# Kernel optimization log

Hardware: AMD Instinct MI355X
Metric: run time of the kernel (lower is better)

## Reference

```python
import jax, jax.numpy as jnp
import numpy as np

NUM_CLASSES = 21
THRESH = 0.5
NEGPOS = 3
VAR0, VAR1 = 0.1, 0.2
FEAT = 19
N_ANCH = 9
B = 256
NUM_OBJS = 12
P = FEAT * FEAT * N_ANCH  # 3249


def make_priors():
    # 19x19 grid, 3 scales x 3 aspect ratios (1, 2, 1/2) -> 9 anchors/cell, center form
    cxy = (np.arange(FEAT, dtype=np.float32) + 0.5) / FEAT
    cx, cy = np.meshgrid(cxy, cxy, indexing='ij')  # [19,19]
    scales = np.array([0.1, 0.2, 0.35], dtype=np.float32)
    ratios = np.array([1.0, 2.0, 0.5], dtype=np.float32)
    w = (scales[:, None] * np.sqrt(ratios)[None, :]).reshape(-1)  # [9]
    h = (scales[:, None] / np.sqrt(ratios)[None, :]).reshape(-1)
    cx = np.broadcast_to(cx[:, :, None], (FEAT, FEAT, N_ANCH))
    cy = np.broadcast_to(cy[:, :, None], (FEAT, FEAT, N_ANCH))
    w = np.broadcast_to(w[None, None, :], (FEAT, FEAT, N_ANCH))
    h = np.broadcast_to(h[None, None, :], (FEAT, FEAT, N_ANCH))
    pri = np.stack([cx, cy, w, h], axis=-1).reshape(-1, 4)
    return jnp.asarray(np.clip(pri, 1e-3, 1.0))


def setup_inputs() -> dict:
    key = jax.random.key(0)
    k1, k2, k3, k4, k5 = jax.random.split(key, 5)
    loc_data = jax.random.normal(k1, (B, P, 4), dtype=jnp.float32)
    conf_data = jax.random.normal(k2, (B, P, NUM_CLASSES), dtype=jnp.float32)
    priors = make_priors()
    xy = jax.random.uniform(k3, (B, NUM_OBJS, 2), minval=0.05, maxval=0.65)
    wh = jax.random.uniform(k4, (B, NUM_OBJS, 2), minval=0.05, maxval=0.30)
    labels = jax.random.randint(k5, (B, NUM_OBJS), 0, NUM_CLASSES - 1).astype(jnp.float32)
    targets = jnp.concatenate([xy, xy + wh, labels[..., None]], axis=-1)  # [B,O,5]
    return {"loc_data": loc_data, "conf_data": conf_data, "priors": priors, "targets": targets}


def point_form(boxes):  # (cx,cy,w,h) -> (x1,y1,x2,y2)
    return jnp.concatenate([boxes[:, :2] - boxes[:, 2:] / 2,
                            boxes[:, :2] + boxes[:, 2:] / 2], axis=1)


def jaccard(a, b):  # a: [n,4], b: [m,4] point form -> [n,m]
    lt = jnp.maximum(a[:, None, :2], b[None, :, :2])
    rb = jnp.minimum(a[:, None, 2:], b[None, :, 2:])
    inter = jnp.prod(jnp.clip(rb - lt, 0.0, None), axis=-1)
    area_a = jnp.prod(a[:, 2:] - a[:, :2], axis=-1)
    area_b = jnp.prod(b[:, 2:] - b[:, :2], axis=-1)
    return inter / (area_a[:, None] + area_b[None, :] - inter)


def encode(matched, priors):  # matched point-form [P,4], priors center-form [P,4]
    g_cxcy = ((matched[:, :2] + matched[:, 2:]) / 2 - priors[:, :2]) / (VAR0 * priors[:, 2:])
    g_wh = jnp.log((matched[:, 2:] - matched[:, :2]) / priors[:, 2:]) / VAR1
    return jnp.concatenate([g_cxcy, g_wh], axis=1)


def match_one(truths, labels, priors, priors_pt):
    overlaps = jaccard(truths, priors_pt)          # [O,P]
    best_prior_idx = jnp.argmax(overlaps, axis=1)  # [O]
    best_truth_ov = jnp.max(overlaps, axis=0)      # [P]
    best_truth_idx = jnp.argmax(overlaps, axis=0)  # [P]
    best_truth_ov = best_truth_ov.at[best_prior_idx].set(2.0)
    best_truth_idx = best_truth_idx.at[best_prior_idx].set(jnp.arange(truths.shape[0]))
    matches = truths[best_truth_idx]               # [P,4]
    conf = labels[best_truth_idx] + 1
    conf = jnp.where(best_truth_ov < THRESH, 0, conf)
    return encode(matches, priors), conf


def reference(loc_data, conf_data, priors, targets):
    truths = targets[:, :, :4]
    labels = targets[:, :, 4].astype(jnp.int32)
    priors_pt = point_form(priors)
    loc_t, conf_t = jax.vmap(lambda t, l: match_one(t, l, priors, priors_pt))(truths, labels)
    loc_t = jax.lax.stop_gradient(loc_t)
    conf_t = jax.lax.stop_gradient(conf_t)

    pos = conf_t > 0                                               # [B,P]
    # smooth L1 (sum) over matched priors
    d = loc_data - loc_t
    ad = jnp.abs(d)
    sl1 = jnp.where(ad < 1.0, 0.5 * d * d, ad - 0.5)
    loss_l = jnp.sum(sl1 * pos[..., None].astype(sl1.dtype))

    # per-prior CE = logsumexp - logit[target]
    lse = jax.nn.logsumexp(conf_data, axis=-1)                     # [B,P]
    gathered = jnp.take_along_axis(conf_data, conf_t[..., None], axis=2)[..., 0]
    ce = lse - gathered                                            # [B,P]

    # hard negative mining: double argsort rank of neg losses
    loss_c_mine = jnp.where(pos, 0.0, ce)
    loss_idx = jnp.argsort(-loss_c_mine, axis=1)
    idx_rank = jnp.argsort(loss_idx, axis=1)
    num_pos = jnp.sum(pos, axis=1, keepdims=True)                  # [B,1]
    num_neg = jnp.minimum(NEGPOS * num_pos, P - 1)
    neg = idx_rank < num_neg

    sel = pos | neg
    loss_c = jnp.sum(jnp.where(sel, ce, 0.0))

    have_centerloss = jnp.max(sel.reshape(B, FEAT, FEAT, N_ANCH), axis=3).reshape(-1)
    conf_t_featuremap = jnp.max(conf_t.reshape(B, FEAT, FEAT, N_ANCH), axis=3).reshape(-1)

    N = jnp.sum(num_pos).astype(loc_data.dtype)
    return loss_l / N, loss_c / N, conf_t_featuremap, have_centerloss
```

## Files before the change

kernel.cpp:

```cpp
#include <hip/hip_runtime.h>
#include <math.h>

#pragma clang fp contract(off)

#define BB      256
#define PP      3249
#define NCLS    21
#define NOBJ    12
#define CELLS   361
#define THRESH_ 0.5f

typedef float vf4 __attribute__((ext_vector_type(4), aligned(4)));


__global__ __launch_bounds__(1024) void fused_kernel(
    const float* __restrict__ loc, const float* __restrict__ conf,
    const float* __restrict__ priors, const float* __restrict__ targets,
    int* __restrict__ numpos, double* __restrict__ lossl,
    double* __restrict__ lossc, float* __restrict__ out)
{
    const int b = blockIdx.x, tid = threadIdx.x;
    const int lane = tid & 63, wid = tid >> 6;

    __shared__ float s_tx1[NOBJ], s_ty1[NOBJ], s_tx2[NOBJ], s_ty2[NOBJ];
    __shared__ float s_area_t[NOBJ];
    __shared__ int   s_label[NOBJ];
    __shared__ float s_bov[PP];
    __shared__ short s_bidx[PP];
    __shared__ int   s_bpi[NOBJ];
    __shared__ float s_wov[NOBJ][16];
    __shared__ int   s_widx[NOBJ][16];
    __shared__ unsigned long long s_key[PP];
    __shared__ unsigned char s_ct[PP];
    __shared__ unsigned char s_sel[PP];
    __shared__ int s_hist[256];
    __shared__ int s_chosen, s_knext, s_nneg;
    __shared__ double s_pl[16];
    __shared__ int    s_pn[16];
    __shared__ double s_pc[16];

    if (tid < NOBJ) {
        const float* t = targets + ((size_t)b * NOBJ + tid) * 5;
        float x1 = t[0], y1 = t[1], x2 = t[2], y2 = t[3];
        s_tx1[tid] = x1; s_ty1[tid] = y1; s_tx2[tid] = x2; s_ty2[tid] = y2;
        s_label[tid] = (int)t[4];
        s_area_t[tid] = (x2 - x1) * (y2 - y1);
    }
    __syncthreads();

    float l_bov[NOBJ];
    int   l_bidx[NOBJ];
#pragma unroll
    for (int j = 0; j < NOBJ; ++j) { l_bov[j] = -1.0f; l_bidx[j] = 0x7FFFFFFF; }

    for (int p = tid; p < PP; p += 1024) {
        float cx = priors[4*p+0], cy = priors[4*p+1], w = priors[4*p+2], h = priors[4*p+3];
        float px1 = cx - w / 2.0f, py1 = cy - h / 2.0f;
        float px2 = cx + w / 2.0f, py2 = cy + h / 2.0f;
        float area_p = (px2 - px1) * (py2 - py1);
        float bov = -1.0f; int bidx = 0;
#pragma unroll
        for (int j = 0; j < NOBJ; ++j) {
            float ltx = fmaxf(s_tx1[j], px1);
            float lty = fmaxf(s_ty1[j], py1);
            float rbx = fminf(s_tx2[j], px2);
            float rby = fminf(s_ty2[j], py2);
            float iw = fmaxf(rbx - ltx, 0.0f);
            float ih = fmaxf(rby - lty, 0.0f);
            float inter = iw * ih;
            float iou = inter / ((s_area_t[j] + area_p) - inter);
            if (iou > bov) { bov = iou; bidx = j; }
            if (iou > l_bov[j]) { l_bov[j] = iou; l_bidx[j] = p; }
        }
        s_bov[p] = bov;
        s_bidx[p] = (short)bidx;
    }

#pragma unroll
    for (int j = 0; j < NOBJ; ++j) {
        float ov = l_bov[j]; int ix = l_bidx[j];
#pragma unroll
        for (int off = 32; off > 0; off >>= 1) {
            float ov2 = __shfl_xor(ov, off);
            int   ix2 = __shfl_xor(ix, off);
            if (ov2 > ov || (ov2 == ov && ix2 < ix)) { ov = ov2; ix = ix2; }
        }
        if (lane == 0) { s_wov[j][wid] = ov; s_widx[j][wid] = ix; }
    }
    __syncthreads();
    if (tid < NOBJ) {
        float ov = s_wov[tid][0]; int ix = s_widx[tid][0];
#pragma unroll
        for (int w2 = 1; w2 < 16; ++w2) {
            float ov2 = s_wov[tid][w2]; int ix2 = s_widx[tid][w2];
            if (ov2 > ov || (ov2 == ov && ix2 < ix)) { ov = ov2; ix = ix2; }
        }
        s_bpi[tid] = ix;
    }
    __syncthreads();

    int my_pos = 0;
    double my_lossl = 0.0;
    const float* confb = conf + (size_t)b * PP * NCLS;
    for (int p = tid; p < PP; p += 1024) {
        int jov = -1;
#pragma unroll
        for (int j = 0; j < NOBJ; ++j) if (s_bpi[j] == p) jov = j;
        int idx; float ov;
        if (jov >= 0) { idx = jov; ov = 2.0f; }
        else          { idx = (int)s_bidx[p]; ov = s_bov[p]; }
        int c = (ov < THRESH_) ? 0 : (s_label[idx] + 1);
        s_ct[p] = (unsigned char)c;

        const float* cd = confb + (size_t)p * NCLS;
        const vf4* cd4 = (const vf4*)cd;
        float rw[NCLS];
#pragma unroll
        for (int v = 0; v < 5; ++v) {
            vf4 q = cd4[v];
            rw[4*v+0] = q[0]; rw[4*v+1] = q[1]; rw[4*v+2] = q[2]; rw[4*v+3] = q[3];
        }
        rw[20] = cd[20];

        float m = rw[0];
#pragma unroll
        for (int k = 1; k < NCLS; ++k) m = fmaxf(m, rw[k]);
        float s = 0.0f;
#pragma unroll
        for (int k = 0; k < NCLS; ++k) s += expf(rw[k] - m);
        float cdc = rw[0];
#pragma unroll
        for (int k = 1; k < NCLS; ++k) if (c == k) cdc = rw[k];
        float ce = (logf(s) + m) - cdc;

        float v = (c > 0) ? 0.0f : ce;
        s_key[p] = ((unsigned long long)__float_as_uint(v) << 32)
                 | (unsigned int)(0xFFFFFFFFu - (unsigned int)p);
        s_bov[p] = ce;

        if (c > 0) {
            ++my_pos;
            float cx = priors[4*p+0], cy = priors[4*p+1], w = priors[4*p+2], h = priors[4*p+3];
            float m0 = s_tx1[idx], m1 = s_ty1[idx], m2 = s_tx2[idx], m3 = s_ty2[idx];
            float g0 = ((m0 + m2) / 2.0f - cx) / (0.1f * w);
            float g1 = ((m1 + m3) / 2.0f - cy) / (0.1f * h);
            float g2 = logf((m2 - m0) / w) / 0.2f;
            float g3 = logf((m3 - m1) / h) / 0.2f;
            const float* ld = loc + ((size_t)b * PP + p) * 4;
            float d0 = ld[0] - g0, d1 = ld[1] - g1, d2 = ld[2] - g2, d3 = ld[3] - g3;
            float a0 = fabsf(d0), a1 = fabsf(d1), a2 = fabsf(d2), a3 = fabsf(d3);
            my_lossl += (double)((a0 < 1.0f) ? 0.5f * d0 * d0 : a0 - 0.5f);
            my_lossl += (double)((a1 < 1.0f) ? 0.5f * d1 * d1 : a1 - 0.5f);
            my_lossl += (double)((a2 < 1.0f) ? 0.5f * d2 * d2 : a2 - 0.5f);
            my_lossl += (double)((a3 < 1.0f) ? 0.5f * d3 * d3 : a3 - 0.5f);
        }
    }
#pragma unroll
    for (int off = 32; off > 0; off >>= 1) {
        my_lossl += __shfl_down(my_lossl, off);
        my_pos   += __shfl_down(my_pos, off);
    }
    if (lane == 0) { s_pl[wid] = my_lossl; s_pn[wid] = my_pos; }
    __syncthreads();
    if (tid == 0) {
        double L = 0.0; int n = 0;
#pragma unroll
        for (int w2 = 0; w2 < 16; ++w2) { L += s_pl[w2]; n += s_pn[w2]; }
        lossl[b] = L; numpos[b] = n;
        s_nneg = min(3 * n, PP - 1);
    }
    __syncthreads();

    const int ds[6] = {56, 48, 40, 32, 8, 0};
    unsigned long long prefix = 0ull, pmask = 0ull;
    int kk = s_nneg;
#pragma unroll
    for (int ri = 0; ri < 6; ++ri) {
        const int d = ds[ri];
        if (tid < 256) s_hist[tid] = 0;
        __syncthreads();
        for (int i = tid; i < PP; i += 1024) {
            unsigned long long key = s_key[i];
            if ((key & pmask) == prefix)
                atomicAdd(&s_hist[(int)((key >> d) & 0xFF)], 1);
        }
        __syncthreads();
        if (tid < 64) {
            int h0 = s_hist[4*lane+0], h1 = s_hist[4*lane+1];
            int h2 = s_hist[4*lane+2], h3 = s_hist[4*lane+3];
            int ls = h0 + h1 + h2 + h3;
            int x = ls;
#pragma unroll
            for (int off = 1; off < 64; off <<= 1) {
                int y = __shfl_down(x, off);
                if (lane + off < 64) x += y;
            }
            int excl = x - ls;
            int cb3 = excl;
            int cb2 = cb3 + h3;
            int cb1 = cb2 + h2;
            int cb0 = cb1 + h1;
            if (cb3 < kk && kk <= cb3 + h3) { s_chosen = 4*lane+3; s_knext = kk - cb3; }
            if (cb2 < kk && kk <= cb2 + h2) { s_chosen = 4*lane+2; s_knext = kk - cb2; }
            if (cb1 < kk && kk <= cb1 + h1) { s_chosen = 4*lane+1; s_knext = kk - cb1; }
            if (cb0 < kk && kk <= cb0 + h0) { s_chosen = 4*lane+0; s_knext = kk - cb0; }
        }
        __syncthreads();
        prefix |= ((unsigned long long)(unsigned int)s_chosen) << d;
        pmask  |= 0xFFull << d;
        kk = s_knext;
        if (d == 32) { prefix |= 0xFFFF0000ull; pmask |= 0xFFFF0000ull; }
        __syncthreads();
    }
    const unsigned long long kth = prefix;

    double my_c = 0.0;
    for (int p = tid; p < PP; p += 1024) {
        int c = s_ct[p];
        bool sel = (c > 0) || (s_key[p] >= kth);
        s_sel[p] = sel ? 1 : 0;
        if (sel) my_c += (double)s_bov[p];
    }
    __syncthreads();

    for (int cI = tid; cI < CELLS; cI += 1024) {
        int mc = 0, hv = 0;
#pragma unroll
        for (int a = 0; a < 9; ++a) {
            int p = cI * 9 + a;
            int cv = s_ct[p];
            mc = (cv > mc) ? cv : mc;
            hv |= s_sel[p];
        }
        out[2 + (size_t)b * CELLS + cI] = (float)mc;
        out[2 + (size_t)BB * CELLS + (size_t)b * CELLS + cI] = (float)hv;
    }

#pragma unroll
    for (int off = 32; off > 0; off >>= 1) my_c += __shfl_down(my_c, off);
    if (lane == 0) s_pc[wid] = my_c;
    __syncthreads();
    if (tid == 0) {
        double L = 0.0;
#pragma unroll
        for (int w2 = 0; w2 < 16; ++w2) L += s_pc[w2];
        lossc[b] = L;
    }
}

__global__ __launch_bounds__(256) void finalize_kernel(
    const int* __restrict__ numpos, const double* __restrict__ lossl,
    const double* __restrict__ lossc, float* __restrict__ out)
{
    __shared__ double s_l[256], s_c[256];
    __shared__ int s_n[256];
    int tid = threadIdx.x;
    s_n[tid] = numpos[tid];
    s_l[tid] = lossl[tid];
    s_c[tid] = lossc[tid];
    __syncthreads();
    for (int s = 128; s > 0; s >>= 1) {
        if (tid < s) { s_n[tid] += s_n[tid + s]; s_l[tid] += s_l[tid + s]; s_c[tid] += s_c[tid + s]; }
        __syncthreads();
    }
    if (tid == 0) {
        double N = (double)s_n[0];
        out[0] = (float)(s_l[0] / N);
        out[1] = (float)(s_c[0] / N);
    }
}

extern "C" void kernel_launch(void* const* d_in, const int* in_sizes, int n_in,
                              void* d_out, int out_size, void* d_ws, size_t ws_size,
                              hipStream_t stream) {
    const float* loc     = (const float*)d_in[0];
    const float* conf    = (const float*)d_in[1];
    const float* priors  = (const float*)d_in[2];
    const float* targets = (const float*)d_in[3];
    float* out = (float*)d_out;

    double* ws_lossl  = (double*)d_ws;
    double* ws_lossc  = ws_lossl + BB;
    int*    ws_numpos = (int*)(ws_lossc + BB);

    hipLaunchKernelGGL(fused_kernel, dim3(BB), dim3(1024), 0, stream,
                       loc, conf, priors, targets, ws_numpos, ws_lossl, ws_lossc, out);
    hipLaunchKernelGGL(finalize_kernel, dim3(1), dim3(256), 0, stream,
                       ws_numpos, ws_lossl, ws_lossc, out);
}
```

Baseline: 138.5 us.

## Split log-sum-exp into a grid-wide kernel and warp-aggregate histogram atomics

Moves the per-prior log-sum-exp over the 21 class logits out of the 256-block fused kernel into a separate kernel with one thread per prior, spread across thousands of blocks. The fused kernel then only gathers the target logit and reads the precomputed LSE. The goal is to stream the large conf tensor with much more parallelism than one block per image allows. The radix-select histogram now combines same-bin increments within a wavefront using ballots before the shared atomic, and double-buffers the histogram to drop one barrier per round. Object indices are also cached in registers. The cost is an extra launch, a workspace round trip for the LSE values, and a scattered re-read of one logit per prior.

After: 150.6 us. 1.09x slower.

```diff
diff --git a/kernel.cpp b/kernel.cpp
--- a/kernel.cpp
+++ b/kernel.cpp
@@ -13,9 +13,34 @@
 typedef float vf4 __attribute__((ext_vector_type(4), aligned(4)));
 
 
+__global__ __launch_bounds__(256) void lse_kernel(
+    const float* __restrict__ conf, float* __restrict__ lse_out)
+{
+    int idx = blockIdx.x * 256 + threadIdx.x;
+    if (idx >= BB * PP) return;
+    const float* cd = conf + (size_t)idx * NCLS;
+    const vf4* cd4 = (const vf4*)cd;
+    float rw[NCLS];
+#pragma unroll
+    for (int v = 0; v < 5; ++v) {
+        vf4 q = cd4[v];
+        rw[4*v+0] = q[0]; rw[4*v+1] = q[1]; rw[4*v+2] = q[2]; rw[4*v+3] = q[3];
+    }
+    rw[20] = cd[20];
+
+    float m = rw[0];
+#pragma unroll
+    for (int k = 1; k < NCLS; ++k) m = fmaxf(m, rw[k]);
+    float s = 0.0f;
+#pragma unroll
+    for (int k = 0; k < NCLS; ++k) s += expf(rw[k] - m);
+    lse_out[idx] = logf(s) + m;
+}
+
 __global__ __launch_bounds__(1024) void fused_kernel(
     const float* __restrict__ loc, const float* __restrict__ conf,
     const float* __restrict__ priors, const float* __restrict__ targets,
+    const float* __restrict__ lse_in,
     int* __restrict__ numpos, double* __restrict__ lossl,
     double* __restrict__ lossc, float* __restrict__ out)
 {
@@ -33,7 +58,7 @@
     __shared__ unsigned long long s_key[PP];
     __shared__ unsigned char s_ct[PP];
     __shared__ unsigned char s_sel[PP];
-    __shared__ int s_hist[256];
+    __shared__ int s_hist[2][256];
     __shared__ int s_chosen, s_knext, s_nneg;
     __shared__ double s_pl[16];
     __shared__ int    s_pn[16];
@@ -99,39 +124,27 @@
     }
     __syncthreads();
 
+    int bpi[NOBJ];
+#pragma unroll
+    for (int j = 0; j < NOBJ; ++j) bpi[j] = s_bpi[j];
+
     int my_pos = 0;
     double my_lossl = 0.0;
     const float* confb = conf + (size_t)b * PP * NCLS;
+    const float* lseb  = lse_in + (size_t)b * PP;
     for (int p = tid; p < PP; p += 1024) {
         int jov = -1;
 #pragma unroll
-        for (int j = 0; j < NOBJ; ++j) if (s_bpi[j] == p) jov = j;
+        for (int j = 0; j < NOBJ; ++j) if (bpi[j] == p) jov = j;
         int idx; float ov;
         if (jov >= 0) { idx = jov; ov = 2.0f; }
         else          { idx = (int)s_bidx[p]; ov = s_bov[p]; }
         int c = (ov < THRESH_) ? 0 : (s_label[idx] + 1);
         s_ct[p] = (unsigned char)c;
 
-        const float* cd = confb + (size_t)p * NCLS;
-        const vf4* cd4 = (const vf4*)cd;
-        float rw[NCLS];
-#pragma unroll
-        for (int v = 0; v < 5; ++v) {
-            vf4 q = cd4[v];
-            rw[4*v+0] = q[0]; rw[4*v+1] = q[1]; rw[4*v+2] = q[2]; rw[4*v+3] = q[3];
-        }
-        rw[20] = cd[20];
-
-        float m = rw[0];
-#pragma unroll
-        for (int k = 1; k < NCLS; ++k) m = fmaxf(m, rw[k]);
-        float s = 0.0f;
-#pragma unroll
-        for (int k = 0; k < NCLS; ++k) s += expf(rw[k] - m);
-        float cdc = rw[0];
-#pragma unroll
-        for (int k = 1; k < NCLS; ++k) if (c == k) cdc = rw[k];
-        float ce = (logf(s) + m) - cdc;
+        float lse = lseb[p];
+        float cdc = confb[(size_t)p * NCLS + c];
+        float ce  = lse - cdc;
 
         float v = (c > 0) ? 0.0f : ce;
         s_key[p] = ((unsigned long long)__float_as_uint(v) << 32)
@@ -161,6 +174,7 @@
         my_pos   += __shfl_down(my_pos, off);
     }
     if (lane == 0) { s_pl[wid] = my_lossl; s_pn[wid] = my_pos; }
+    if (tid < 512) ((int*)s_hist)[tid] = 0;
     __syncthreads();
     if (tid == 0) {
         double L = 0.0; int n = 0;
@@ -177,17 +191,24 @@
 #pragma unroll
     for (int ri = 0; ri < 6; ++ri) {
         const int d = ds[ri];
-        if (tid < 256) s_hist[tid] = 0;
-        __syncthreads();
+        int* hist = s_hist[ri & 1];
         for (int i = tid; i < PP; i += 1024) {
             unsigned long long key = s_key[i];
-            if ((key & pmask) == prefix)
-                atomicAdd(&s_hist[(int)((key >> d) & 0xFF)], 1);
+            bool active = ((key & pmask) == prefix);
+            unsigned bin = (unsigned)((key >> d) & 0xFF);
+            unsigned long long mm = __ballot(active);
+#pragma unroll
+            for (int bit = 0; bit < 8; ++bit) {
+                unsigned long long bb = __ballot(active && ((bin >> bit) & 1));
+                mm &= ((bin >> bit) & 1) ? bb : ~bb;
+            }
+            if (active && (__ffsll((unsigned long long)mm) - 1 == lane))
+                atomicAdd(&hist[bin], (int)__popcll(mm));
         }
         __syncthreads();
         if (tid < 64) {
-            int h0 = s_hist[4*lane+0], h1 = s_hist[4*lane+1];
-            int h2 = s_hist[4*lane+2], h3 = s_hist[4*lane+3];
+            int h0 = hist[4*lane+0], h1 = hist[4*lane+1];
+            int h2 = hist[4*lane+2], h3 = hist[4*lane+3];
             int ls = h0 + h1 + h2 + h3;
             int x = ls;
 #pragma unroll
@@ -204,13 +225,14 @@
             if (cb2 < kk && kk <= cb2 + h2) { s_chosen = 4*lane+2; s_knext = kk - cb2; }
             if (cb1 < kk && kk <= cb1 + h1) { s_chosen = 4*lane+1; s_knext = kk - cb1; }
             if (cb0 < kk && kk <= cb0 + h0) { s_chosen = 4*lane+0; s_knext = kk - cb0; }
+        } else if (tid < 64 + 256) {
+            s_hist[(ri + 1) & 1][tid - 64] = 0;
         }
         __syncthreads();
         prefix |= ((unsigned long long)(unsigned int)s_chosen) << d;
         pmask  |= 0xFFull << d;
         kk = s_knext;
         if (d == 32) { prefix |= 0xFFFF0000ull; pmask |= 0xFFFF0000ull; }
-        __syncthreads();
     }
     const unsigned long long kth = prefix;
 
@@ -282,9 +304,13 @@
     double* ws_lossl  = (double*)d_ws;
     double* ws_lossc  = ws_lossl + BB;
     int*    ws_numpos = (int*)(ws_lossc + BB);
-
+    float*  ws_lse    = (float*)(ws_numpos + BB);
+
+    hipLaunchKernelGGL(lse_kernel, dim3((BB * PP) / 256), dim3(256), 0, stream,
+                       conf, ws_lse);
     hipLaunchKernelGGL(fused_kernel, dim3(BB), dim3(1024), 0, stream,
-                       loc, conf, priors, targets, ws_numpos, ws_lossl, ws_lossc, out);
+                       loc, conf, priors, targets, ws_lse,
+                       ws_numpos, ws_lossl, ws_lossc, out);
     hipLaunchKernelGGL(finalize_kernel, dim3(1), dim3(256), 0, stream,
                        ws_numpos, ws_lossl, ws_lossc, out);
 }
```

## Overlap conf loads with IoU, shrink radix select to 32-bit keys

Applied to the files above, without the earlier changes.

Conf rows and priors are now loaded up front so their global-memory latency overlaps the IoU matching, and the per-prior logsumexp is precomputed into shared memory. The target-class logit is then gathered with a single load. The 64-bit radix select over eight 8-bit passes is replaced by a 32-bit key select using 12-bit histograms built with ballot-aggregated atomics, stopping early once the chosen bin holds a single element. Ties are resolved by a separate index pass, and selection is fused into the per-cell output loop. This adds a lot of shared memory and register pressure, which may limit occupancy.

New measurement: 141.9 us. 2.4% more time.

```diff
diff --git a/kernel.cpp b/kernel.cpp
--- a/kernel.cpp
+++ b/kernel.cpp
@@ -9,11 +9,79 @@
 #define NOBJ    12
 #define CELLS   361
 #define THRESH_ 0.5f
+#define HB      4096
 
 typedef float vf4 __attribute__((ext_vector_type(4), aligned(4)));
 
 
-__global__ __launch_bounds__(1024) void fused_kernel(
+struct Row { vf4 a, b, c, d, e; float f; };
+
+__device__ __forceinline__ Row load_row(const float* cd) {
+    const vf4* q = (const vf4*)cd;
+    Row r;
+    r.a = q[0]; r.b = q[1]; r.c = q[2]; r.d = q[3]; r.e = q[4];
+    r.f = cd[20];
+    return r;
+}
+
+__device__ __forceinline__ float lse21(const Row& r) {
+    float m = r.a[0];
+    m = fmaxf(m, r.a[1]); m = fmaxf(m, r.a[2]); m = fmaxf(m, r.a[3]);
+    m = fmaxf(m, r.b[0]); m = fmaxf(m, r.b[1]); m = fmaxf(m, r.b[2]); m = fmaxf(m, r.b[3]);
+    m = fmaxf(m, r.c[0]); m = fmaxf(m, r.c[1]); m = fmaxf(m, r.c[2]); m = fmaxf(m, r.c[3]);
+    m = fmaxf(m, r.d[0]); m = fmaxf(m, r.d[1]); m = fmaxf(m, r.d[2]); m = fmaxf(m, r.d[3]);
+    m = fmaxf(m, r.e[0]); m = fmaxf(m, r.e[1]); m = fmaxf(m, r.e[2]); m = fmaxf(m, r.e[3]);
+    m = fmaxf(m, r.f);
+    float s = 0.0f;
+    s += expf(r.a[0]-m); s += expf(r.a[1]-m); s += expf(r.a[2]-m); s += expf(r.a[3]-m);
+    s += expf(r.b[0]-m); s += expf(r.b[1]-m); s += expf(r.b[2]-m); s += expf(r.b[3]-m);
+    s += expf(r.c[0]-m); s += expf(r.c[1]-m); s += expf(r.c[2]-m); s += expf(r.c[3]-m);
+    s += expf(r.d[0]-m); s += expf(r.d[1]-m); s += expf(r.d[2]-m); s += expf(r.d[3]-m);
+    s += expf(r.e[0]-m); s += expf(r.e[1]-m); s += expf(r.e[2]-m); s += expf(r.e[3]-m);
+    s += expf(r.f-m);
+    return logf(s) + m;
+}
+
+template <int NBITS>
+__device__ __forceinline__ void scan_hist(const unsigned* key_arr, int* hist,
+                                          unsigned prefix, unsigned pmask,
+                                          int shift, int tid, int lane) {
+    for (int i = tid; i < PP; i += 1024) {
+        unsigned key = key_arr[i];
+        bool active = ((key & pmask) == prefix);
+        unsigned bin = (key >> shift) & ((1u << NBITS) - 1u);
+        unsigned long long mm = __ballot(active);
+#pragma unroll
+        for (int bit = 0; bit < NBITS; ++bit) {
+            unsigned long long bb = __ballot(active && ((bin >> bit) & 1));
+            mm &= ((bin >> bit) & 1) ? bb : ~bb;
+        }
+        if (active && (__ffsll((unsigned long long)mm) - 1 == lane))
+            atomicAdd(&hist[bin], (int)__popcll(mm));
+    }
+}
+
+__device__ __forceinline__ void pick_bin(const int* hist, int nbins, int kv, int lane,
+                                         int* s_chosen, int* s_knext, int* s_cnt) {
+    const int per = nbins >> 6;
+    const int base = lane * per;
+    int ls = 0;
+    for (int k = 0; k < per; ++k) ls += hist[base + k];
+    int x = ls;
+#pragma unroll
+    for (int off = 1; off < 64; off <<= 1) {
+        int y = __shfl_down(x, off);
+        if (lane + off < 64) x += y;
+    }
+    int cum = x - ls;
+    for (int k = per - 1; k >= 0; --k) {
+        int h = hist[base + k];
+        if (cum < kv && kv <= cum + h) { *s_chosen = base + k; *s_knext = kv - cum; *s_cnt = h; }
+        cum += h;
+    }
+}
+
+__global__ __launch_bounds__(1024, 4) void fused_kernel(
     const float* __restrict__ loc, const float* __restrict__ conf,
     const float* __restrict__ priors, const float* __restrict__ targets,
     int* __restrict__ numpos, double* __restrict__ lossl,
@@ -27,14 +95,16 @@
     __shared__ int   s_label[NOBJ];
     __shared__ float s_bov[PP];
     __shared__ short s_bidx[PP];
+    __shared__ float s_lse[PP];
+    __shared__ float s_c0[PP];
+    __shared__ unsigned s_key[PP];
+    __shared__ unsigned char s_ct[PP];
     __shared__ int   s_bpi[NOBJ];
     __shared__ float s_wov[NOBJ][16];
     __shared__ int   s_widx[NOBJ][16];
-    __shared__ unsigned long long s_key[PP];
-    __shared__ unsigned char s_ct[PP];
-    __shared__ unsigned char s_sel[PP];
-    __shared__ int s_hist[256];
-    __shared__ int s_chosen, s_knext, s_nneg;
+    __shared__ int s_hist[2][HB];
+    __shared__ int s_chosen, s_knext, s_cnt, s_nneg;
+    __shared__ unsigned s_f;
     __shared__ double s_pl[16];
     __shared__ int    s_pn[16];
     __shared__ double s_pc[16];
@@ -48,13 +118,23 @@
     }
     __syncthreads();
 
+    const float* confb = conf + (size_t)b * PP * NCLS;
+    const int p0 = tid, p1 = tid + 1024, p2 = tid + 2048, p3 = tid + 3072;
+    const bool h3 = (p3 < PP);
+
+    vf4 pr0 = *(const vf4*)(priors + 4 * p0);
+    vf4 pr1 = *(const vf4*)(priors + 4 * p1);
+    vf4 pr2 = *(const vf4*)(priors + 4 * p2);
+    vf4 pr3; if (h3) pr3 = *(const vf4*)(priors + 4 * p3);
+    Row ra = load_row(confb + (size_t)p0 * NCLS);
+
     float l_bov[NOBJ];
     int   l_bidx[NOBJ];
 #pragma unroll
     for (int j = 0; j < NOBJ; ++j) { l_bov[j] = -1.0f; l_bidx[j] = 0x7FFFFFFF; }
 
-    for (int p = tid; p < PP; p += 1024) {
-        float cx = priors[4*p+0], cy = priors[4*p+1], w = priors[4*p+2], h = priors[4*p+3];
+    auto iou_body = [&](vf4 prr, int p) {
+        float cx = prr[0], cy = prr[1], w = prr[2], h = prr[3];
         float px1 = cx - w / 2.0f, py1 = cy - h / 2.0f;
         float px2 = cx + w / 2.0f, py2 = cy + h / 2.0f;
         float area_p = (px2 - px1) * (py2 - py1);
@@ -74,7 +154,11 @@
         }
         s_bov[p] = bov;
         s_bidx[p] = (short)bidx;
-    }
+    };
+    iou_body(pr0, p0);
+    iou_body(pr1, p1);
+    iou_body(pr2, p2);
+    if (h3) iou_body(pr3, p3);
 
 #pragma unroll
     for (int j = 0; j < NOBJ; ++j) {
@@ -87,7 +171,18 @@
         }
         if (lane == 0) { s_wov[j][wid] = ov; s_widx[j][wid] = ix; }
     }
-    __syncthreads();
+
+    {
+        Row rb = load_row(confb + (size_t)p1 * NCLS);
+        s_lse[p0] = lse21(ra); s_c0[p0] = ra.a[0];
+        Row rc = load_row(confb + (size_t)p2 * NCLS);
+        s_lse[p1] = lse21(rb); s_c0[p1] = rb.a[0];
+        Row rd; if (h3) rd = load_row(confb + (size_t)p3 * NCLS);
+        s_lse[p2] = lse21(rc); s_c0[p2] = rc.a[0];
+        if (h3) { s_lse[p3] = lse21(rd); s_c0[p3] = rd.a[0]; }
+    }
+    __syncthreads();
+
     if (tid < NOBJ) {
         float ov = s_wov[tid][0]; int ix = s_widx[tid][0];
 #pragma unroll
@@ -99,43 +194,28 @@
     }
     __syncthreads();
 
+    int bpi[NOBJ];
+#pragma unroll
+    for (int j = 0; j < NOBJ; ++j) bpi[j] = s_bpi[j];
+
     int my_pos = 0;
     double my_lossl = 0.0;
-    const float* confb = conf + (size_t)b * PP * NCLS;
     for (int p = tid; p < PP; p += 1024) {
         int jov = -1;
 #pragma unroll
-        for (int j = 0; j < NOBJ; ++j) if (s_bpi[j] == p) jov = j;
+        for (int j = 0; j < NOBJ; ++j) if (bpi[j] == p) jov = j;
         int idx; float ov;
         if (jov >= 0) { idx = jov; ov = 2.0f; }
         else          { idx = (int)s_bidx[p]; ov = s_bov[p]; }
         int c = (ov < THRESH_) ? 0 : (s_label[idx] + 1);
         s_ct[p] = (unsigned char)c;
 
-        const float* cd = confb + (size_t)p * NCLS;
-        const vf4* cd4 = (const vf4*)cd;
-        float rw[NCLS];
-#pragma unroll
-        for (int v = 0; v < 5; ++v) {
-            vf4 q = cd4[v];
-            rw[4*v+0] = q[0]; rw[4*v+1] = q[1]; rw[4*v+2] = q[2]; rw[4*v+3] = q[3];
-        }
-        rw[20] = cd[20];
-
-        float m = rw[0];
-#pragma unroll
-        for (int k = 1; k < NCLS; ++k) m = fmaxf(m, rw[k]);
-        float s = 0.0f;
-#pragma unroll
-        for (int k = 0; k < NCLS; ++k) s += expf(rw[k] - m);
-        float cdc = rw[0];
-#pragma unroll
-        for (int k = 1; k < NCLS; ++k) if (c == k) cdc = rw[k];
-        float ce = (logf(s) + m) - cdc;
+        float lse = s_lse[p];
+        float cdc = (c == 0) ? s_c0[p] : confb[(size_t)p * NCLS + c];
+        float ce  = lse - cdc;
 
         float v = (c > 0) ? 0.0f : ce;
-        s_key[p] = ((unsigned long long)__float_as_uint(v) << 32)
-                 | (unsigned int)(0xFFFFFFFFu - (unsigned int)p);
+        s_key[p] = __float_as_uint(v);
         s_bov[p] = ce;
 
         if (c > 0) {
@@ -161,7 +241,13 @@
         my_pos   += __shfl_down(my_pos, off);
     }
     if (lane == 0) { s_pl[wid] = my_lossl; s_pn[wid] = my_pos; }
-    __syncthreads();
+    for (int k = tid; k < 2 * HB; k += 1024) ((int*)s_hist)[k] = 0;
+    __syncthreads();
+
+    unsigned prefix = 0u, pmask = 0u, fstar = 0u;
+    int ptie = 0x7FFFFFFF;
+    bool resolved = false;
+
     if (tid == 0) {
         double L = 0.0; int n = 0;
 #pragma unroll
@@ -169,68 +255,79 @@
         lossl[b] = L; numpos[b] = n;
         s_nneg = min(3 * n, PP - 1);
     }
-    __syncthreads();
-
-    const int ds[6] = {56, 48, 40, 32, 8, 0};
-    unsigned long long prefix = 0ull, pmask = 0ull;
-    int kk = s_nneg;
-#pragma unroll
-    for (int ri = 0; ri < 6; ++ri) {
-        const int d = ds[ri];
-        if (tid < 256) s_hist[tid] = 0;
-        __syncthreads();
+    scan_hist<12>(s_key, s_hist[0], 0u, 0u, 20, tid, lane);
+    __syncthreads();
+    if (tid < 64) pick_bin(s_hist[0], HB, s_nneg, lane, &s_chosen, &s_knext, &s_cnt);
+    else { for (int k = tid - 64; k < HB; k += 960) s_hist[1][k] = 0; }
+    __syncthreads();
+    prefix = ((unsigned)s_chosen) << 20; pmask = 0xFFF00000u;
+    if (s_cnt == 1) {
         for (int i = tid; i < PP; i += 1024) {
-            unsigned long long key = s_key[i];
-            if ((key & pmask) == prefix)
-                atomicAdd(&s_hist[(int)((key >> d) & 0xFF)], 1);
-        }
-        __syncthreads();
-        if (tid < 64) {
-            int h0 = s_hist[4*lane+0], h1 = s_hist[4*lane+1];
-            int h2 = s_hist[4*lane+2], h3 = s_hist[4*lane+3];
-            int ls = h0 + h1 + h2 + h3;
-            int x = ls;
-#pragma unroll
-            for (int off = 1; off < 64; off <<= 1) {
-                int y = __shfl_down(x, off);
-                if (lane + off < 64) x += y;
+            unsigned key = s_key[i];
+            if ((key & pmask) == prefix) s_f = key;
+        }
+        __syncthreads();
+        fstar = s_f; resolved = true;
+    }
+
+    if (!resolved) {
+        scan_hist<12>(s_key, s_hist[1], prefix, pmask, 8, tid, lane);
+        __syncthreads();
+        if (tid < 64) pick_bin(s_hist[1], HB, s_knext, lane, &s_chosen, &s_knext, &s_cnt);
+        else { for (int k = tid - 64; k < HB; k += 960) s_hist[0][k] = 0; }
+        __syncthreads();
+        prefix |= ((unsigned)s_chosen) << 8; pmask |= 0x000FFF00u;
+        if (s_cnt == 1) {
+            for (int i = tid; i < PP; i += 1024) {
+                unsigned key = s_key[i];
+                if ((key & pmask) == prefix) s_f = key;
             }
-            int excl = x - ls;
-            int cb3 = excl;
-            int cb2 = cb3 + h3;
-            int cb1 = cb2 + h2;
-            int cb0 = cb1 + h1;
-            if (cb3 < kk && kk <= cb3 + h3) { s_chosen = 4*lane+3; s_knext = kk - cb3; }
-            if (cb2 < kk && kk <= cb2 + h2) { s_chosen = 4*lane+2; s_knext = kk - cb2; }
-            if (cb1 < kk && kk <= cb1 + h1) { s_chosen = 4*lane+1; s_knext = kk - cb1; }
-            if (cb0 < kk && kk <= cb0 + h0) { s_chosen = 4*lane+0; s_knext = kk - cb0; }
-        }
-        __syncthreads();
-        prefix |= ((unsigned long long)(unsigned int)s_chosen) << d;
-        pmask  |= 0xFFull << d;
-        kk = s_knext;
-        if (d == 32) { prefix |= 0xFFFF0000ull; pmask |= 0xFFFF0000ull; }
-        __syncthreads();
-    }
-    const unsigned long long kth = prefix;
+            __syncthreads();
+            fstar = s_f; resolved = true;
+        }
+    }
+
+    if (!resolved) {
+        scan_hist<8>(s_key, s_hist[0], prefix, pmask, 0, tid, lane);
+        __syncthreads();
+        if (tid < 64) pick_bin(s_hist[0], 256, s_knext, lane, &s_chosen, &s_knext, &s_cnt);
+        else { for (int k = tid - 64; k < HB; k += 960) s_hist[1][k] = 0; }
+        __syncthreads();
+        prefix |= (unsigned)s_chosen;
+        fstar = prefix;
+        if (s_knext < s_cnt) {
+            int* hist = s_hist[1];
+            for (int i = tid; i < PP; i += 1024) {
+                bool active = (s_key[i] == fstar);
+                unsigned bin = 4095u - (unsigned)i;
+                unsigned long long mm = __ballot(active);
+#pragma unroll
+                for (int bit = 0; bit < 12; ++bit) {
+                    unsigned long long bb = __ballot(active && ((bin >> bit) & 1));
+                    mm &= ((bin >> bit) & 1) ? bb : ~bb;
+                }
+                if (active && (__ffsll((unsigned long long)mm) - 1 == lane))
+                    atomicAdd(&hist[bin], (int)__popcll(mm));
+            }
+            __syncthreads();
+            if (tid < 64) pick_bin(hist, HB, s_knext, lane, &s_chosen, &s_knext, &s_cnt);
+            __syncthreads();
+            ptie = 4095 - s_chosen;
+        }
+    }
 
     double my_c = 0.0;
-    for (int p = tid; p < PP; p += 1024) {
-        int c = s_ct[p];
-        bool sel = (c > 0) || (s_key[p] >= kth);
-        s_sel[p] = sel ? 1 : 0;
-        if (sel) my_c += (double)s_bov[p];
-    }
-    __syncthreads();
-
     for (int cI = tid; cI < CELLS; cI += 1024) {
         int mc = 0, hv = 0;
 #pragma unroll
         for (int a = 0; a < 9; ++a) {
             int p = cI * 9 + a;
             int cv = s_ct[p];
+            unsigned v = s_key[p];
+            bool sel = (cv > 0) || (v > fstar) || (v == fstar && p <= ptie);
             mc = (cv > mc) ? cv : mc;
-            hv |= s_sel[p];
+            hv |= sel ? 1 : 0;
+            if (sel) my_c += (double)s_bov[p];
         }
         out[2 + (size_t)b * CELLS + cI] = (float)mc;
         out[2 + (size_t)BB * CELLS + (size_t)b * CELLS + cI] = (float)hv;
```
